# Kernel optimization log

Hardware: AMD Instinct MI355X
Metric: run time of the kernel (lower is better)

The kernel has to match this reference:

```python
import jax, jax.numpy as jnp
import numpy as np

NEG_INF = -1e30

def setup_inputs() -> dict:
    key = jax.random.key(0)
    kx, kq, kk, kv = jax.random.split(key, 4)
    B, T, C, H = 4, 4096, 2048, 128
    x = jax.random.normal(kx, (B, T, C), dtype=jnp.float32)
    Wq = jax.random.normal(kq, (C, H), dtype=jnp.float32) * (C ** -0.5)
    Wk = jax.random.normal(kk, (C, H), dtype=jnp.float32) * (C ** -0.5)
    Wv = jax.random.normal(kv, (C, H), dtype=jnp.float32) * (C ** -0.5)
    return {"x": x, "Wq": Wq, "Wk": Wk, "Wv": Wv}

def reference(x, Wq, Wk, Wv):
    B, T, C = x.shape
    q = x @ Wq  # [B, T, H]
    k = x @ Wk
    v = x @ Wv
    # NOTE: original scales by channels**-0.5 (n_embd), not head_size**-0.5
    scale = C ** -0.5
    wei = jnp.einsum('bqh,bkh->bqk', q, k) * scale  # [B, T, T]
    causal = jnp.tril(jnp.ones((T, T), dtype=bool))
    wei = jnp.where(causal, wei, NEG_INF)
    wei = jax.nn.softmax(wei, axis=-1)
    return jnp.einsum('bqk,bkh->bqh', wei, v)
```

## Files before the change

kernel.cpp:

```cpp
#include <hip/hip_runtime.h>


typedef __attribute__((ext_vector_type(8))) short s8v;
typedef __attribute__((ext_vector_type(4))) float f4v;

__device__ __forceinline__ unsigned short f2bf(float f) {
  unsigned int b = __float_as_uint(f);
  b += 0x7FFFu + ((b >> 16) & 1u);
  return (unsigned short)(b >> 16);
}
__device__ __forceinline__ unsigned int pk2bf(float lo, float hi) {
  return (unsigned int)f2bf(lo) | ((unsigned int)f2bf(hi) << 16);
}

#define SCALE_QK 0.02209708691207961f

__global__ void prep_wt(const float* __restrict__ Wq, const float* __restrict__ Wk,
                        const float* __restrict__ Wv, unsigned short* __restrict__ WT) {
  int e = blockIdx.x * 256 + threadIdx.x;
  int m = e >> 18;
  int r = e & 262143;
  int c = r >> 7, h = r & 127;
  const float* W = (m == 0) ? Wq : (m == 1) ? Wk : Wv;
  float v = W[r];
  if (m == 0) v *= SCALE_QK;
  WT[m * 262144 + h * 2048 + c] = f2bf(v);
}

__global__ __launch_bounds__(512, 1) void proj_kernel(
    const float* __restrict__ x, const unsigned short* __restrict__ WT,
    unsigned short* __restrict__ Qo, unsigned short* __restrict__ Ko,
    unsigned short* __restrict__ VTo)
{
  __shared__ __align__(16) char psmem[116736];
  unsigned short* scr = (unsigned short*)psmem;

  const int tid = threadIdx.x;
  const int w = tid >> 6, lane = tid & 63;
  const int l15 = lane & 15, g = lane >> 4;
  const int wr = w >> 2, wc = w & 3;
  const int rowbase = blockIdx.x * 64;

  f4v acc[12];
  #pragma unroll
  for (int n = 0; n < 12; ++n) acc[n] = (f4v){0.f, 0.f, 0.f, 0.f};

  const int arow = tid >> 3;
  const int akc  = (tid & 7) * 16;
  const float* xsrc = x + (size_t)(rowbase + arow) * 2048 + (tid & 7) * 8;
  const char* WTb = (const char*)WT;

#define STAGE_B(dst_, k0_)                                                     \
  {                                                                            \
    _Pragma("unroll")                                                          \
    for (int p = 0; p < 6; ++p) {                                              \
      const int off = tid * 16 + p * 8192;                                     \
      const int row = off >> 7, chunk = off & 127;                             \
      __builtin_amdgcn_global_load_lds(                                        \
        (const __attribute__((address_space(1))) void*)(                       \
            WTb + (size_t)row * 4096 + (size_t)(k0_) * 2 +                     \
            (chunk ^ ((row & 7) << 4))),                                       \
        (__attribute__((address_space(3))) void*)((dst_) + off), 16, 0, 0);    \
    }                                                                          \
  }

#define WRITE_A(dst_, aa_, ab_)                                                \
  {                                                                            \
    s8v t_;                                                                    \
    _Pragma("unroll")                                                          \
    for (int i = 0; i < 4; ++i) { t_[i] = (short)f2bf(aa_[i]);                 \
                                  t_[i + 4] = (short)f2bf(ab_[i]); }           \
    *(s8v*)((dst_) + arow * 144 + akc) = t_;                                   \
  }

#define COMPUTE(SEL)                                                           \
  {                                                                            \
    const char* Bb = psmem + (SEL) * 49152;                                    \
    const char* Ab = psmem + 98304 + (SEL) * 9216;                             \
    s8v af[2][2], bfr[6][2];                                                   \
    _Pragma("unroll")                                                          \
    for (int mi = 0; mi < 2; ++mi)                                             \
      _Pragma("unroll")                                                        \
      for (int kk = 0; kk < 2; ++kk)                                           \
        af[mi][kk] = *(const s8v*)(Ab + (32 * wr + 16 * mi + l15) * 144 +      \
                                   kk * 64 + g * 16);                          \
    _Pragma("unroll")                                                          \
    for (int nl = 0; nl < 6; ++nl) {                                           \
      const int row = 96 * wc + 16 * nl + l15;                                 \
      _Pragma("unroll")                                                        \
      for (int kk = 0; kk < 2; ++kk)                                           \
        bfr[nl][kk] = *(const s8v*)(Bb + row * 128 +                           \
                       ((kk * 64 + g * 16) ^ ((l15 & 7) << 4)));               \
    }                                                                          \
    __builtin_amdgcn_s_setprio(1);                                             \
    _Pragma("unroll")                                                          \
    for (int kk = 0; kk < 2; ++kk)                                             \
      _Pragma("unroll")                                                        \
      for (int mi = 0; mi < 2; ++mi)                                           \
        _Pragma("unroll")                                                      \
        for (int nl = 0; nl < 6; ++nl)                                         \
          acc[mi * 6 + nl] = __builtin_amdgcn_mfma_f32_16x16x32_bf16(          \
              af[mi][kk], bfr[nl][kk], acc[mi * 6 + nl], 0, 0, 0);             \
    __builtin_amdgcn_s_setprio(0);                                             \
  }

#define PBODY(SEL, K0, XA, XB, DOX, WN)                                        \
  {                                                                            \
    if ((K0) + 64 < 2048) {                                                    \
      STAGE_B(psmem + ((SEL) ^ 1) * 49152, (K0) + 64)                          \
    }                                                                          \
    __builtin_amdgcn_sched_barrier(0);      \
    if ((K0) + 64 < 2048) {                                                    \
      WRITE_A(psmem + 98304 + ((SEL) ^ 1) * 9216, XA, XB)                      \
    }                                                                          \
    if (DOX) {                                                                 \
      XA = *(const f4v*)(xsrc + (K0) + 192);                                   \
      XB = *(const f4v*)(xsrc + (K0) + 196);                                   \
    }                                                                          \
    COMPUTE(SEL)                                                               \
    asm volatile("s_waitcnt lgkmcnt(0)" ::: "memory");                         \
    asm volatile("s_waitcnt vmcnt(" #WN ")" ::: "memory");                     \
    __builtin_amdgcn_s_barrier();                                              \
    __builtin_amdgcn_sched_barrier(0);                                         \
  }

  f4v xe_a = *(const f4v*)(xsrc);
  f4v xe_b = *(const f4v*)(xsrc + 4);
  STAGE_B(psmem, 0)
  __builtin_amdgcn_sched_barrier(0);
  f4v xo_a = *(const f4v*)(xsrc + 64);
  f4v xo_b = *(const f4v*)(xsrc + 68);
  WRITE_A(psmem + 98304, xe_a, xe_b)
  xe_a = *(const f4v*)(xsrc + 128);
  xe_b = *(const f4v*)(xsrc + 132);
  asm volatile("s_waitcnt lgkmcnt(0)" ::: "memory");
  asm volatile("s_waitcnt vmcnt(4)" ::: "memory");
  __builtin_amdgcn_s_barrier();
  __builtin_amdgcn_sched_barrier(0);

  for (int it = 0; it < 14; ++it) {
    const int k0 = it * 128;
    PBODY(0, k0, xo_a, xo_b, 1, 2)
    PBODY(1, k0 + 64, xe_a, xe_b, 1, 2)
  }
  PBODY(0, 1792, xo_a, xo_b, 1, 2)
  PBODY(1, 1856, xe_a, xe_b, 0, 0)
  PBODY(0, 1920, xo_a, xo_b, 0, 0)
  COMPUTE(1)
#undef PBODY
#undef STAGE_B
#undef WRITE_A
#undef COMPUTE

  #pragma unroll
  for (int mi = 0; mi < 2; ++mi) {
    #pragma unroll
    for (int nl = 0; nl < 6; ++nl) {
      const int colg = 96 * wc + 16 * nl + l15;
      const int m = colg >> 7;
      const int h = colg & 127;
      const f4v a = acc[mi * 6 + nl];
      if (m < 2) {
        unsigned short* dst = (m == 0) ? Qo : Ko;
        #pragma unroll
        for (int r = 0; r < 4; ++r) {
          const int t = rowbase + 32 * wr + 16 * mi + 4 * g + r;
          dst[(size_t)t * 128 + h] = f2bf(a[r]);
        }
      } else {
        #pragma unroll
        for (int r = 0; r < 4; ++r) {
          const int tl = 32 * wr + 16 * mi + 4 * g + r;
          scr[h * 72 + tl] = f2bf(a[r]);
        }
      }
    }
  }
  __syncthreads();
  {
    const int b   = rowbase >> 12;
    const int tg0 = rowbase & 4095;
    const int h    = tid >> 2;
    const int toff = (tid & 3) * 16;
    unsigned short* dst = VTo + (size_t)(b * 128 + h) * 4096 + tg0 + toff;
    *(s8v*)(dst)     = *(const s8v*)(&scr[h * 72 + toff]);
    *(s8v*)(dst + 8) = *(const s8v*)(&scr[h * 72 + toff + 8]);
  }
}

__global__ __launch_bounds__(256, 2) void attn_kernel(
    const unsigned short* __restrict__ Q, const unsigned short* __restrict__ K,
    const unsigned short* __restrict__ VT, float* __restrict__ out)
{
  __shared__ __align__(16) char smem[71168];
  unsigned short* plds = (unsigned short*)(smem + 65536);
  float* mlp = (float*)(smem + 70656);

  const int tid  = threadIdx.x;
  const int w    = tid >> 6;
  const int lane = tid & 63;
  const int l15 = lane & 15, g = lane >> 4;

  const int bid = blockIdx.x;
  const int i8  = bid & 255;
  const int j   = i8 >> 2;
  const int s   = (bid < 256) ? (127 - j) : j;
  const int b   = i8 & 3;
  const int qb = s * 32;
  const int roff = (w >> 1) * 16, half = w & 1;
  const int ntiles = (qb + 95) >> 6;

  const char* Kg = (const char*)(K  + (size_t)b * 4096 * 128);
  const char* Vg = (const char*)(VT + (size_t)b * 128 * 4096);
  const unsigned short* Qb = Q + (size_t)b * 4096 * 128;

  s8v qf[4];
  #pragma unroll
  for (int kk = 0; kk < 4; ++kk)
    qf[kk] = *(const s8v*)(Qb + (size_t)(qb + roff + l15) * 128 + kk * 32 + g * 8);

  f4v o[8];
  #pragma unroll
  for (int n = 0; n < 8; ++n) o[n] = (f4v){0.f, 0.f, 0.f, 0.f};
  float mrun = -1e30f, lrun = 0.f;

  const int off0 = tid * 16;

#define STAGE(Kl_, kvb_)                                                       \
  {                                                                            \
    char* Kl = (Kl_);                                                          \
    _Pragma("unroll")                                                          \
    for (int p = 0; p < 4; ++p) {                                              \
      const int off = off0 + p * 4096;                                         \
      const int ks = off ^ (((off >> 8) & 7) << 4);                            \
      __builtin_amdgcn_global_load_lds(                                        \
        (const __attribute__((address_space(1))) void*)(Kg + (size_t)(kvb_) * 256 + ks), \
        (__attribute__((address_space(3))) void*)(Kl + off), 16, 0, 0);        \
    }                                                                          \
    _Pragma("unroll")                                                          \
    for (int p = 0; p < 4; ++p) {                                              \
      const int off = off0 + p * 4096;                                         \
      const int h = off >> 7;                                                  \
      const int cs = (off & 127) ^ ((h & 7) << 4);                             \
      __builtin_amdgcn_global_load_lds(                                        \
        (const __attribute__((address_space(1))) void*)(Vg + (size_t)h * 8192 + (size_t)(kvb_) * 2 + cs), \
        (__attribute__((address_space(3))) void*)(Kl + 16384 + off), 16, 0, 0); \
    }                                                                          \
  }

  STAGE(smem, 0)
  __syncthreads();

  int cur = 0;
  for (int it = 0; it < ntiles; ++it) {
    const int kvb = it * 64;
    if (it + 1 < ntiles) STAGE(smem + (cur ^ 1) * 32768, kvb + 64)

    const char* Kl = smem + cur * 32768;
    const char* Vl = Kl + 16384;
    s8v kf[2][4];
    #pragma unroll
    for (int t2 = 0; t2 < 2; ++t2) {
      const int row = half * 32 + t2 * 16 + l15;
      #pragma unroll
      for (int kk = 0; kk < 4; ++kk)
        kf[t2][kk] = *(const s8v*)(Kl + ((row * 256 + kk * 64 + g * 16) ^ ((l15 & 7) << 4)));
    }
    s8v vf[8];
    #pragma unroll
    for (int n = 0; n < 8; ++n) {
      const int row = n * 16 + l15;
      vf[n] = *(const s8v*)(Vl + ((row * 128 + half * 64 + g * 16) ^ ((l15 & 7) << 4)));
    }
    f4v sc[2];
    sc[0] = (f4v){0.f, 0.f, 0.f, 0.f};
    sc[1] = (f4v){0.f, 0.f, 0.f, 0.f};
    __builtin_amdgcn_s_setprio(1);
    #pragma unroll
    for (int kk = 0; kk < 4; ++kk) {
      sc[0] = __builtin_amdgcn_mfma_f32_16x16x32_bf16(kf[0][kk], qf[kk], sc[0], 0, 0, 0);
      sc[1] = __builtin_amdgcn_mfma_f32_16x16x32_bf16(kf[1][kk], qf[kk], sc[1], 0, 0, 0);
    }
    __builtin_amdgcn_s_setprio(0);
    if (it == ntiles - 1) {
      const int qrow = qb + roff + l15;
      #pragma unroll
      for (int t2 = 0; t2 < 2; ++t2)
        #pragma unroll
        for (int r = 0; r < 4; ++r) {
          const int kv = kvb + half * 32 + 16 * t2 + 4 * g + r;
          if (kv > qrow) sc[t2][r] = -1e30f;
        }
    }
    float v = fmaxf(fmaxf(fmaxf(sc[0][0], sc[0][1]), fmaxf(sc[0][2], sc[0][3])),
                    fmaxf(fmaxf(sc[1][0], sc[1][1]), fmaxf(sc[1][2], sc[1][3])));
    v = fmaxf(v, __shfl_xor(v, 16));
    v = fmaxf(v, __shfl_xor(v, 32));
    if (__any(v > mrun + 4.0f)) {
      const float mnew = fmaxf(mrun, v);
      const float corr = __expf(mrun - mnew);
      mrun = mnew;
      lrun *= corr;
      #pragma unroll
      for (int n = 0; n < 8; ++n)
        #pragma unroll
        for (int r = 0; r < 4; ++r) o[n][r] *= corr;
    }
    f4v p0, p1;
    #pragma unroll
    for (int r = 0; r < 4; ++r) {
      p0[r] = __expf(sc[0][r] - mrun);
      p1[r] = __expf(sc[1][r] - mrun);
    }
    lrun += (p0[0] + p0[1]) + (p0[2] + p0[3]) + (p1[0] + p1[1]) + (p1[2] + p1[3]);
    unsigned short* pw = plds + w * 640;
    *(unsigned int*)(&pw[l15 * 40 + 4 * g])          = pk2bf(p0[0], p0[1]);
    *(unsigned int*)(&pw[l15 * 40 + 4 * g + 2])      = pk2bf(p0[2], p0[3]);
    *(unsigned int*)(&pw[l15 * 40 + 16 + 4 * g])     = pk2bf(p1[0], p1[1]);
    *(unsigned int*)(&pw[l15 * 40 + 16 + 4 * g + 2]) = pk2bf(p1[2], p1[3]);
    const s8v pf = *(const s8v*)(pw + l15 * 40 + g * 8);
    __builtin_amdgcn_s_setprio(1);
    #pragma unroll
    for (int n = 0; n < 8; ++n)
      o[n] = __builtin_amdgcn_mfma_f32_16x16x32_bf16(vf[n], pf, o[n], 0, 0, 0);
    __builtin_amdgcn_s_setprio(0);

    __syncthreads();
    cur ^= 1;
  }
#undef STAGE

  float lt = lrun;
  lt += __shfl_xor(lt, 16);
  lt += __shfl_xor(lt, 32);
  if (g == 0) {
    mlp[(w * 16 + l15) * 2 + 0] = mrun;
    mlp[(w * 16 + l15) * 2 + 1] = lt;
  }
  float* ol = (float*)smem;
  #pragma unroll
  for (int n = 0; n < 8; ++n)
    *(f4v*)(&ol[(w * 16 + l15) * 132 + 16 * n + 4 * g]) = o[n];
  __syncthreads();

  {
    const int st  = tid >> 7;
    const int t7  = tid & 127;
    const int row = t7 >> 3;
    const int hb  = (t7 & 7) * 16;
    const int wA = 2 * st, wB = 2 * st + 1;
    const float m0 = mlp[(wA * 16 + row) * 2], l0 = mlp[(wA * 16 + row) * 2 + 1];
    const float m1 = mlp[(wB * 16 + row) * 2], l1 = mlp[(wB * 16 + row) * 2 + 1];
    const float M  = fmaxf(m0, m1);
    const float w0 = __expf(m0 - M), w1 = __expf(m1 - M);
    const float inv = 1.0f / (w0 * l0 + w1 * l1);
    float* dst = out + (size_t)(b * 4096 + qb + 16 * st + row) * 128 + hb;
    #pragma unroll
    for (int j4 = 0; j4 < 4; ++j4) {
      const f4v a = *(const f4v*)(&ol[(wA * 16 + row) * 132 + hb + 4 * j4]);
      const f4v c = *(const f4v*)(&ol[(wB * 16 + row) * 132 + hb + 4 * j4]);
      f4v res;
      #pragma unroll
      for (int jj = 0; jj < 4; ++jj) res[jj] = (w0 * a[jj] + w1 * c[jj]) * inv;
      *(f4v*)(dst + 4 * j4) = res;
    }
  }
}

extern "C" void kernel_launch(void* const* d_in, const int* in_sizes, int n_in,
                              void* d_out, int out_size, void* d_ws, size_t ws_size,
                              hipStream_t stream) {
  const float* x  = (const float*)d_in[0];
  const float* Wq = (const float*)d_in[1];
  const float* Wk = (const float*)d_in[2];
  const float* Wv = (const float*)d_in[3];

  unsigned short* WT = (unsigned short*)d_ws;
  unsigned short* Q  = (unsigned short*)((char*)d_ws + 1572864);
  unsigned short* K  = (unsigned short*)((char*)d_ws + 5767168);
  unsigned short* VT = (unsigned short*)((char*)d_ws + 9961472);
  float* out = (float*)d_out;

  prep_wt<<<3072, 256, 0, stream>>>(Wq, Wk, Wv, WT);
  proj_kernel<<<256, 512, 0, stream>>>(x, WT, Q, K, VT);
  attn_kernel<<<512, 256, 0, stream>>>(Q, K, VT, out);
}
```

Before: 111.3 us.

## Shrink projection tile to 32 rows and read weights directly from global

The projection kernel drops from 64-row tiles with 8 waves to 32-row tiles with 4 waves. It now launches 512 blocks instead of 256, which fills more CUs. The weight tile is no longer staged through a double-buffered LDS area via global_load_lds. Each wave now reads its B fragments straight from global/L2 memory, so LDS use falls from about 114KB to 10KB and occupancy rises. The cost is that weight reads are no longer shared through LDS, which doubles global weight traffic per output row and puts global-load latency directly in front of the MFMAs.

After: 175.3 us. 1.58x slower.

```diff
diff --git a/kernel.cpp b/kernel.cpp
--- a/kernel.cpp
+++ b/kernel.cpp
@@ -27,42 +27,28 @@
   WT[m * 262144 + h * 2048 + c] = f2bf(v);
 }
 
-__global__ __launch_bounds__(512, 1) void proj_kernel(
+__global__ __launch_bounds__(256) void proj_kernel(
     const float* __restrict__ x, const unsigned short* __restrict__ WT,
     unsigned short* __restrict__ Qo, unsigned short* __restrict__ Ko,
     unsigned short* __restrict__ VTo)
 {
-  __shared__ __align__(16) char psmem[116736];
+  __shared__ __align__(16) char psmem[10240];
   unsigned short* scr = (unsigned short*)psmem;
 
   const int tid = threadIdx.x;
-  const int w = tid >> 6, lane = tid & 63;
+  const int wc  = tid >> 6;
+  const int lane = tid & 63;
   const int l15 = lane & 15, g = lane >> 4;
-  const int wr = w >> 2, wc = w & 3;
-  const int rowbase = blockIdx.x * 64;
+  const int rowbase = blockIdx.x * 32;
 
   f4v acc[12];
   #pragma unroll
   for (int n = 0; n < 12; ++n) acc[n] = (f4v){0.f, 0.f, 0.f, 0.f};
 
   const int arow = tid >> 3;
-  const int akc  = (tid & 7) * 16;
-  const float* xsrc = x + (size_t)(rowbase + arow) * 2048 + (tid & 7) * 8;
-  const char* WTb = (const char*)WT;
-
-#define STAGE_B(dst_, k0_)                                                     \
-  {                                                                            \
-    _Pragma("unroll")                                                          \
-    for (int p = 0; p < 6; ++p) {                                              \
-      const int off = tid * 16 + p * 8192;                                     \
-      const int row = off >> 7, chunk = off & 127;                             \
-      __builtin_amdgcn_global_load_lds(                                        \
-        (const __attribute__((address_space(1))) void*)(                       \
-            WTb + (size_t)row * 4096 + (size_t)(k0_) * 2 +                     \
-            (chunk ^ ((row & 7) << 4))),                                       \
-        (__attribute__((address_space(3))) void*)((dst_) + off), 16, 0, 0);    \
-    }                                                                          \
-  }
+  const int ach  = tid & 7;
+  const float* xsrc = x + (size_t)(rowbase + arow) * 2048 + ach * 8;
+  const unsigned short* Wbase = WT + (size_t)(96 * wc + l15) * 2048 + g * 8;
 
 #define WRITE_A(dst_, aa_, ab_)                                                \
   {                                                                            \
@@ -70,28 +56,31 @@
     _Pragma("unroll")                                                          \
     for (int i = 0; i < 4; ++i) { t_[i] = (short)f2bf(aa_[i]);                 \
                                   t_[i + 4] = (short)f2bf(ab_[i]); }           \
-    *(s8v*)((dst_) + arow * 144 + akc) = t_;                                   \
-  }
-
-#define COMPUTE(SEL)                                                           \
+    *(s8v*)((dst_) + arow * 144 + ach * 16) = t_;                              \
+  }
+
+#define PBODY(SEL, K0, XA, XB, DOW, DOX)                                       \
   {                                                                            \
-    const char* Bb = psmem + (SEL) * 49152;                                    \
-    const char* Ab = psmem + 98304 + (SEL) * 9216;                             \
-    s8v af[2][2], bfr[6][2];                                                   \
+    if (DOW) { WRITE_A(psmem + ((SEL) ^ 1) * 4608, XA, XB) }                   \
+    if (DOX) {                                                                 \
+      XA = *(const f4v*)(xsrc + (K0) + 192);                                   \
+      XB = *(const f4v*)(xsrc + (K0) + 196);                                   \
+    }                                                                          \
+    s8v bfr[6][2];                                                             \
+    _Pragma("unroll")                                                          \
+    for (int nl = 0; nl < 6; ++nl)                                             \
+      _Pragma("unroll")                                                        \
+      for (int kk = 0; kk < 2; ++kk)                                           \
+        bfr[nl][kk] = *(const s8v*)(Wbase + (size_t)(16 * nl) * 2048 +         \
+                                    (K0) + kk * 32);                           \
+    const char* Ab = psmem + (SEL) * 4608;                                     \
+    s8v af[2][2];                                                              \
     _Pragma("unroll")                                                          \
     for (int mi = 0; mi < 2; ++mi)                                             \
       _Pragma("unroll")                                                        \
       for (int kk = 0; kk < 2; ++kk)                                           \
-        af[mi][kk] = *(const s8v*)(Ab + (32 * wr + 16 * mi + l15) * 144 +      \
+        af[mi][kk] = *(const s8v*)(Ab + (16 * mi + l15) * 144 +                \
                                    kk * 64 + g * 16);                          \
-    _Pragma("unroll")                                                          \
-    for (int nl = 0; nl < 6; ++nl) {                                           \
-      const int row = 96 * wc + 16 * nl + l15;                                 \
-      _Pragma("unroll")                                                        \
-      for (int kk = 0; kk < 2; ++kk)                                           \
-        bfr[nl][kk] = *(const s8v*)(Bb + row * 128 +                           \
-                       ((kk * 64 + g * 16) ^ ((l15 & 7) << 4)));               \
-    }                                                                          \
     __builtin_amdgcn_s_setprio(1);                                             \
     _Pragma("unroll")                                                          \
     for (int kk = 0; kk < 2; ++kk)                                             \
@@ -102,55 +91,32 @@
           acc[mi * 6 + nl] = __builtin_amdgcn_mfma_f32_16x16x32_bf16(          \
               af[mi][kk], bfr[nl][kk], acc[mi * 6 + nl], 0, 0, 0);             \
     __builtin_amdgcn_s_setprio(0);                                             \
-  }
-
-#define PBODY(SEL, K0, XA, XB, DOX, WN)                                        \
-  {                                                                            \
-    if ((K0) + 64 < 2048) {                                                    \
-      STAGE_B(psmem + ((SEL) ^ 1) * 49152, (K0) + 64)                          \
-    }                                                                          \
-    __builtin_amdgcn_sched_barrier(0);      \
-    if ((K0) + 64 < 2048) {                                                    \
-      WRITE_A(psmem + 98304 + ((SEL) ^ 1) * 9216, XA, XB)                      \
-    }                                                                          \
-    if (DOX) {                                                                 \
-      XA = *(const f4v*)(xsrc + (K0) + 192);                                   \
-      XB = *(const f4v*)(xsrc + (K0) + 196);                                   \
-    }                                                                          \
-    COMPUTE(SEL)                                                               \
     asm volatile("s_waitcnt lgkmcnt(0)" ::: "memory");                         \
-    asm volatile("s_waitcnt vmcnt(" #WN ")" ::: "memory");                     \
     __builtin_amdgcn_s_barrier();                                              \
     __builtin_amdgcn_sched_barrier(0);                                         \
   }
 
   f4v xe_a = *(const f4v*)(xsrc);
   f4v xe_b = *(const f4v*)(xsrc + 4);
-  STAGE_B(psmem, 0)
-  __builtin_amdgcn_sched_barrier(0);
   f4v xo_a = *(const f4v*)(xsrc + 64);
   f4v xo_b = *(const f4v*)(xsrc + 68);
-  WRITE_A(psmem + 98304, xe_a, xe_b)
+  WRITE_A(psmem, xe_a, xe_b)
   xe_a = *(const f4v*)(xsrc + 128);
   xe_b = *(const f4v*)(xsrc + 132);
   asm volatile("s_waitcnt lgkmcnt(0)" ::: "memory");
-  asm volatile("s_waitcnt vmcnt(4)" ::: "memory");
   __builtin_amdgcn_s_barrier();
   __builtin_amdgcn_sched_barrier(0);
 
-  for (int it = 0; it < 14; ++it) {
-    const int k0 = it * 128;
-    PBODY(0, k0, xo_a, xo_b, 1, 2)
-    PBODY(1, k0 + 64, xe_a, xe_b, 1, 2)
-  }
-  PBODY(0, 1792, xo_a, xo_b, 1, 2)
-  PBODY(1, 1856, xe_a, xe_b, 0, 0)
-  PBODY(0, 1920, xo_a, xo_b, 0, 0)
-  COMPUTE(1)
+  for (int t = 0; t < 28; t += 2) {
+    PBODY(0, t * 64, xo_a, xo_b, 1, 1)
+    PBODY(1, t * 64 + 64, xe_a, xe_b, 1, 1)
+  }
+  PBODY(0, 1792, xo_a, xo_b, 1, 1)
+  PBODY(1, 1856, xe_a, xe_b, 1, 0)
+  PBODY(0, 1920, xo_a, xo_b, 1, 0)
+  PBODY(1, 1984, xe_a, xe_b, 0, 0)
 #undef PBODY
-#undef STAGE_B
 #undef WRITE_A
-#undef COMPUTE
 
   #pragma unroll
   for (int mi = 0; mi < 2; ++mi) {
@@ -164,14 +130,14 @@
         unsigned short* dst = (m == 0) ? Qo : Ko;
         #pragma unroll
         for (int r = 0; r < 4; ++r) {
-          const int t = rowbase + 32 * wr + 16 * mi + 4 * g + r;
+          const int t = rowbase + mi * 16 + 4 * g + r;
           dst[(size_t)t * 128 + h] = f2bf(a[r]);
         }
       } else {
         #pragma unroll
         for (int r = 0; r < 4; ++r) {
-          const int tl = 32 * wr + 16 * mi + 4 * g + r;
-          scr[h * 72 + tl] = f2bf(a[r]);
+          const int tl = mi * 16 + 4 * g + r;
+          scr[h * 40 + tl] = f2bf(a[r]);
         }
       }
     }
@@ -180,11 +146,11 @@
   {
     const int b   = rowbase >> 12;
     const int tg0 = rowbase & 4095;
-    const int h    = tid >> 2;
-    const int toff = (tid & 3) * 16;
+    const int h    = tid >> 1;
+    const int toff = (tid & 1) * 16;
     unsigned short* dst = VTo + (size_t)(b * 128 + h) * 4096 + tg0 + toff;
-    *(s8v*)(dst)     = *(const s8v*)(&scr[h * 72 + toff]);
-    *(s8v*)(dst + 8) = *(const s8v*)(&scr[h * 72 + toff + 8]);
+    *(s8v*)(dst)     = *(const s8v*)(&scr[h * 40 + toff]);
+    *(s8v*)(dst + 8) = *(const s8v*)(&scr[h * 40 + toff + 8]);
   }
 }
 
@@ -382,6 +348,6 @@
   float* out = (float*)d_out;
 
   prep_wt<<<3072, 256, 0, stream>>>(Wq, Wk, Wv, WT);
-  proj_kernel<<<256, 512, 0, stream>>>(x, WT, Q, K, VT);
+  proj_kernel<<<512, 256, 0, stream>>>(x, WT, Q, K, VT);
   attn_kernel<<<512, 256, 0, stream>>>(Q, K, VT, out);
 }
```
